# Performance work log

Measured on AMD Instinct MI355X. Metric: run time of the kernel, lower is better.

## Reference

```python
import jax, jax.numpy as jnp
import numpy as np

NUM_HEADS = 16
D_MODEL = 1024
HEAD_DIM = D_MODEL // NUM_HEADS
EPS = 1e-6


def setup_inputs() -> dict:
    key = jax.random.key(0)
    ks = jax.random.split(key, 9)
    B, S, D = 4, 8192, D_MODEL
    scale = 1.0 / np.sqrt(D)  # variance_scaling(1.0, fan_in, normal) approx
    inputs_q = jax.random.normal(ks[0], (B, S, D), dtype=jnp.float32)
    Wq = jax.random.normal(ks[1], (D, D), dtype=jnp.float32) * scale
    Wk = jax.random.normal(ks[2], (D, D), dtype=jnp.float32) * scale
    Wv = jax.random.normal(ks[3], (D, D), dtype=jnp.float32) * scale
    Wo = jax.random.normal(ks[4], (D, D), dtype=jnp.float32) * scale
    bq = jnp.zeros((D,), jnp.float32)
    bk = jnp.zeros((D,), jnp.float32)
    bv = jnp.zeros((D,), jnp.float32)
    bo = jnp.zeros((D,), jnp.float32)
    return {"inputs_q": inputs_q, "Wq": Wq, "bq": bq, "Wk": Wk, "bk": bk,
            "Wv": Wv, "bv": bv, "Wo": Wo, "bo": bo}


def _feature_map(x):
    return jax.nn.elu(x) + 1.0


def reference(inputs_q, Wq, bq, Wk, bk, Wv, bv, Wo, bo):
    B, S, D = inputs_q.shape
    H, Dh = NUM_HEADS, HEAD_DIM
    # QKV projections (self-attention: k,v inputs default to q input)
    q = (inputs_q @ Wq + bq).reshape(B, S, H, Dh)
    k = (inputs_q @ Wk + bk).reshape(B, S, H, Dh)
    v = (inputs_q @ Wv + bv).reshape(B, S, H, Dh)
    q = _feature_map(q)
    k = _feature_map(k)
    # KV outer-product accumulation: [B, H, Dh, Dh]
    kv = jnp.einsum('bkhd,bkhm->bhdm', k, v)
    out = jnp.einsum('bqhd,bhdm->bqhm', q, kv)
    # normalizer: q . sum_k(k)
    normalizer = jnp.einsum('bqhd,bkhd->bqh', q, k)
    normalizer = jnp.maximum(normalizer, EPS)
    out = out / normalizer[..., None]
    out = out.reshape(B, S, D)
    return out @ Wo + bo
```

## Files before the change

kernel.cpp:

```cpp
#include <hip/hip_runtime.h>
#include <cstdint>
#include <cstddef>

#define D_MODEL 1024
#define SEQ 8192

typedef __bf16  bf16x8 __attribute__((ext_vector_type(8)));
typedef short   short8 __attribute__((ext_vector_type(8)));
typedef float   f32x4  __attribute__((ext_vector_type(4)));
typedef unsigned short ushort_t;

__device__ __forceinline__ ushort_t f2bf(float f) {
  uint32_t u = __builtin_bit_cast(uint32_t, f);
  u += 0x7FFFu + ((u >> 16) & 1u);
  return (ushort_t)(u >> 16);
}
__device__ __forceinline__ void gll16(const void* g, void* l) {
  __builtin_amdgcn_global_load_lds(
      (const __attribute__((address_space(1))) void*)g,
      (__attribute__((address_space(3))) void*)l, 16, 0, 0);
}

__global__ void k_convert_x(const float* __restrict__ x, ushort_t* __restrict__ xb, int n) {
  int i = (blockIdx.x * 256 + threadIdx.x) * 8;
  if (i >= n) return;
  float4 v0 = *(const float4*)(x + i);
  float4 v1 = *(const float4*)(x + i + 4);
  ushort_t o[8] = { f2bf(v0.x), f2bf(v0.y), f2bf(v0.z), f2bf(v0.w),
                    f2bf(v1.x), f2bf(v1.y), f2bf(v1.z), f2bf(v1.w) };
  *(short8*)(xb + i) = *(const short8*)o;
}

__global__ void k_transpose_w(const float* W0, const float* W1, const float* W2, const float* W3,
                              ushort_t* Tqkv, ushort_t* To) {
  const float* src; ushort_t* dst;
  switch (blockIdx.z) {
    case 0: src = W0; dst = Tqkv; break;
    case 1: src = W1; dst = Tqkv + (size_t)1024 * 1024; break;
    case 2: src = W2; dst = Tqkv + (size_t)2048 * 1024; break;
    default: src = W3; dst = To; break;
  }
  __shared__ float tile[64][65];
  int tx = threadIdx.x;
  int c = tx & 63, r0 = tx >> 6;
  int bx = blockIdx.x * 64, by = blockIdx.y * 64;
  #pragma unroll
  for (int i = 0; i < 16; i++) {
    int r = i * 4 + r0;
    tile[r][c] = src[(size_t)(by + r) * D_MODEL + bx + c];
  }
  __syncthreads();
  #pragma unroll
  for (int i = 0; i < 16; i++) {
    int r = i * 4 + r0;
    dst[(size_t)(bx + r) * D_MODEL + by + c] = f2bf(tile[c][r]);
  }
}

template<int MODE, int NY>
__global__ __launch_bounds__(256) void k_gemm(const ushort_t* __restrict__ A,
                                              const ushort_t* __restrict__ Bt,
                                              const float* __restrict__ b0,
                                              const float* __restrict__ b1,
                                              const float* __restrict__ b2,
                                              ushort_t* __restrict__ o0,
                                              ushort_t* __restrict__ o1,
                                              ushort_t* __restrict__ o2,
                                              float* __restrict__ outf) {
  constexpr int SMEM_BYTES = (MODE == 2) ? 33792 : 32768;
  __shared__ __align__(16) char smem[SMEM_BYTES];
  ushort_t* As = (ushort_t*)smem;
  ushort_t* Bs = (ushort_t*)(smem + 8192);

  const int bid = blockIdx.x;
  const int xb = bid / NY;
  const int yb = bid % NY;
  const int m0 = xb * 128;
  const int n0 = yb * 128;

  const int tid = threadIdx.x;
  const int ln = tid & 63;
  const int w = tid >> 6;
  const int wr = (w >> 1) * 64, wc = (w & 1) * 64;

  const int lr = tid >> 2;
  const int kg = (tid & 3) * 8;
  const ushort_t* gA0 = A + (size_t)(m0 + lr) * D_MODEL + kg;
  const ushort_t* gA1 = gA0 + (size_t)64 * D_MODEL;
  const ushort_t* gB0 = Bt + (size_t)(n0 + lr) * D_MODEL + kg;
  const ushort_t* gB1 = gB0 + (size_t)64 * D_MODEL;

  const int wb = __builtin_amdgcn_readfirstlane(w);
  ushort_t* lA0 = As + wb * 512;
  ushort_t* lA1 = As + 2048 + wb * 512;
  ushort_t* lB0 = Bs + wb * 512;
  ushort_t* lB1 = Bs + 2048 + wb * 512;

  f32x4 acc[4][4];
  #pragma unroll
  for (int i = 0; i < 4; i++)
    #pragma unroll
    for (int j = 0; j < 4; j++) acc[i][j] = (f32x4){0.f, 0.f, 0.f, 0.f};

  const int ar = ln & 15;
  const int aq = (ln >> 4) * 8;

  for (int kt = 0; kt < D_MODEL / 32; kt++) {
    gll16(gA0, lA0); gll16(gA1, lA1);
    gll16(gB0, lB0); gll16(gB1, lB1);
    gA0 += 32; gA1 += 32; gB0 += 32; gB1 += 32;
    __syncthreads();
    bf16x8 a[4], b[4];
    #pragma unroll
    for (int i = 0; i < 4; i++) a[i] = *(const bf16x8*)&As[(wr + i * 16 + ar) * 32 + aq];
    #pragma unroll
    for (int j = 0; j < 4; j++) b[j] = *(const bf16x8*)&Bs[(wc + j * 16 + ar) * 32 + aq];
    #pragma unroll
    for (int i = 0; i < 4; i++)
      #pragma unroll
      for (int j = 0; j < 4; j++)
        acc[i][j] = __builtin_amdgcn_mfma_f32_16x16x32_bf16(a[i], b[j], acc[i][j], 0, 0, 0);
    __syncthreads();
  }

  const int colb = ln & 15;
  const int rowb = (ln >> 4) * 4;

  if (MODE == 0) {
    const int region = yb >> 3;
    const int nl0 = (yb & 7) * 128;
    const float* bias = region == 0 ? b0 : (region == 1 ? b1 : b2);
    ushort_t* gout    = region == 0 ? o0 : (region == 1 ? o1 : o2);
    const bool act = region < 2;
    ushort_t* Cs = (ushort_t*)smem;
    #pragma unroll
    for (int j = 0; j < 4; j++) {
      const int col = wc + j * 16 + colb;
      const float bv_ = bias[nl0 + col];
      #pragma unroll
      for (int i = 0; i < 4; i++) {
        const int rbase = wr + i * 16 + rowb;
        #pragma unroll
        for (int r = 0; r < 4; r++) {
          float v = acc[i][j][r] + bv_;
          if (act) v = (v > 0.f) ? v + 1.f : __expf(v);
          const int row = rbase + r;
          const int cg = col >> 3, co = col & 7;
          Cs[row * 128 + (((cg ^ (row & 15))) << 3) + co] = f2bf(v);
        }
      }
    }
    __syncthreads();
    #pragma unroll
    for (int c = 0; c < 8; c++) {
      const int idx = c * 256 + tid;
      const int row = idx >> 4, cg = idx & 15;
      short8 t = *(const short8*)&Cs[row * 128 + ((cg ^ (row & 15)) << 3)];
      *(short8*)&gout[(size_t)(m0 + row) * D_MODEL + nl0 + cg * 8] = t;
    }
  } else {
    float* Cf = (float*)smem;
    #pragma unroll
    for (int h = 0; h < 2; h++) {
      if (h) __syncthreads();
      if ((wr >> 6) == h) {
        #pragma unroll
        for (int j = 0; j < 4; j++) {
          const int col = wc + j * 16 + colb;
          const float bv_ = b0[n0 + col];
          #pragma unroll
          for (int i = 0; i < 4; i++) {
            const int rl = i * 16 + rowb;
            #pragma unroll
            for (int r = 0; r < 4; r++)
              Cf[(rl + r) * 132 + col] = acc[i][j][r] + bv_;
          }
        }
      }
      __syncthreads();
      #pragma unroll
      for (int c = 0; c < 8; c++) {
        const int idx = c * 256 + tid;
        const int row = idx >> 5, cg = idx & 31;
        float4 t = *(const float4*)&Cf[row * 132 + cg * 4];
        *(float4*)&outf[(size_t)(m0 + h * 64 + row) * D_MODEL + n0 + cg * 4] = t;
      }
    }
  }
}

__global__ __launch_bounds__(256) void k_kv_partial(const ushort_t* __restrict__ kmat,
                                                    const ushort_t* __restrict__ vmat,
                                                    float* __restrict__ part) {
  __shared__ __align__(16) ushort_t sbuf[4][2][2][512];
  const int tid = threadIdx.x, ln = tid & 63, w = tid >> 6;
  const int wb = __builtin_amdgcn_readfirstlane(w);
  const int bh = blockIdx.y, chunk = blockIdx.x;
  const int b = bh >> 4, h = bh & 15;
  const size_t cbase = ((size_t)b * SEQ + chunk * 1024 + w * 256) * D_MODEL + h * 64;
  const ushort_t* gk = kmat + cbase + (size_t)(ln >> 3) * D_MODEL + (ln & 7) * 8;
  const ushort_t* gv = vmat + cbase + (size_t)(ln >> 3) * D_MODEL + (ln & 7) * 8;

  float acc[8][8];
  float ksum[8];
  #pragma unroll
  for (int i = 0; i < 8; i++) { ksum[i] = 0.f;
    #pragma unroll
    for (int j = 0; j < 8; j++) acc[i][j] = 0.f; }

  const int r8 = (ln >> 3) * 8, c8 = (ln & 7) * 8;
  gll16(gk, &sbuf[wb][0][0][0]);
  gll16(gv, &sbuf[wb][0][1][0]);
  gk += 8 * D_MODEL; gv += 8 * D_MODEL;

  for (int bt = 0; bt < 32; bt++) {
    const int p = bt & 1;
    if (bt < 31) {
      gll16(gk, &sbuf[wb][p ^ 1][0][0]);
      gll16(gv, &sbuf[wb][p ^ 1][1][0]);
      gk += 8 * D_MODEL; gv += 8 * D_MODEL;
      __builtin_amdgcn_s_waitcnt(0x0F72);
    } else {
      __builtin_amdgcn_s_waitcnt(0x0F70);
    }
    #pragma unroll
    for (int s = 0; s < 8; s++) {
      short8 kk = *(const short8*)&sbuf[wb][p][0][s * 64 + r8];
      short8 vv = *(const short8*)&sbuf[wb][p][1][s * 64 + c8];
      float ka[8], va[8];
      #pragma unroll
      for (int i = 0; i < 8; i++) {
        ka[i] = __builtin_bit_cast(float, (uint32_t)(ushort_t)kk[i] << 16);
        va[i] = __builtin_bit_cast(float, (uint32_t)(ushort_t)vv[i] << 16);
      }
      #pragma unroll
      for (int i = 0; i < 8; i++) {
        ksum[i] += ka[i];
        #pragma unroll
        for (int j = 0; j < 8; j++) acc[i][j] += ka[i] * va[j];
      }
    }
  }
  float* p0 = part + ((size_t)bh * 32 + chunk * 4 + w) * 4160;
  #pragma unroll
  for (int i = 0; i < 8; i++)
    #pragma unroll
    for (int j = 0; j < 8; j++) p0[(r8 + i) * 64 + c8 + j] = acc[i][j];
  if ((ln & 7) == 0) {
    #pragma unroll
    for (int i = 0; i < 8; i++) p0[4096 + r8 + i] = ksum[i];
  }
}

__global__ void k_kv_reduce(const float* __restrict__ part, ushort_t* __restrict__ kvt) {
  const int bh = blockIdx.x, tid = threadIdx.x;
  const float* p0 = part + (size_t)bh * 32 * 4160;
  for (int idx = tid; idx < 4160; idx += 256) {
    float s = 0.f;
    #pragma unroll 4
    for (int c = 0; c < 32; c++) s += p0[(size_t)c * 4160 + idx];
    ushort_t bf = f2bf(s);
    if (idx < 4096) { int d = idx >> 6, m = idx & 63; kvt[(size_t)bh * 4160 + m * 64 + d] = bf; }
    else            { kvt[(size_t)bh * 4160 + 4096 + (idx - 4096)] = bf; }
  }
}

__global__ __launch_bounds__(256) void k_attn(const ushort_t* __restrict__ qmat,
                                              const ushort_t* __restrict__ kvt,
                                              ushort_t* __restrict__ attn) {
  __shared__ __align__(16) ushort_t kvs[65 * 80];
  __shared__ __align__(16) ushort_t qs[4][64 * 80];
  const int tid = threadIdx.x, ln = tid & 63, w = tid >> 6;
  const int bh = blockIdx.y, b = bh >> 4, h = bh & 15;

  for (int idx = tid; idx < 4160; idx += 256) {
    int m = idx >> 6, d = idx & 63;
    kvs[m * 80 + d] = kvt[(size_t)bh * 4160 + idx];
  }
  const size_t s0 = (size_t)b * SEQ + blockIdx.x * 256 + w * 64;
  #pragma unroll
  for (int c = 0; c < 8; c++) {
    int f = c * 64 + ln;
    int row = f >> 3, dg = (f & 7) * 8;
    short8 t = *(const short8*)&qmat[(s0 + row) * D_MODEL + h * 64 + dg];
    *(short8*)&qs[w][row * 80 + dg] = t;
  }
  __syncthreads();

  const int ar = ln & 15, aq = (ln >> 4) * 8;
  f32x4 acc[4][4], nacc[4];
  #pragma unroll
  for (int i = 0; i < 4; i++) { nacc[i] = (f32x4){0.f, 0.f, 0.f, 0.f};
    #pragma unroll
    for (int j = 0; j < 4; j++) acc[i][j] = (f32x4){0.f, 0.f, 0.f, 0.f}; }

  #pragma unroll
  for (int kk = 0; kk < 2; kk++) {
    const int ko = kk * 32 + aq;
    bf16x8 a[4], bb[4], bn;
    #pragma unroll
    for (int i = 0; i < 4; i++) a[i] = *(const bf16x8*)&qs[w][(i * 16 + ar) * 80 + ko];
    #pragma unroll
    for (int j = 0; j < 4; j++) bb[j] = *(const bf16x8*)&kvs[(j * 16 + ar) * 80 + ko];
    bn = *(const bf16x8*)&kvs[64 * 80 + ko];
    #pragma unroll
    for (int i = 0; i < 4; i++) {
      #pragma unroll
      for (int j = 0; j < 4; j++)
        acc[i][j] = __builtin_amdgcn_mfma_f32_16x16x32_bf16(a[i], bb[j], acc[i][j], 0, 0, 0);
      nacc[i] = __builtin_amdgcn_mfma_f32_16x16x32_bf16(a[i], bn, nacc[i], 0, 0, 0);
    }
  }

  const int colb = ln & 15, rowb = (ln >> 4) * 4;
  #pragma unroll
  for (int i = 0; i < 4; i++) {
    #pragma unroll
    for (int r = 0; r < 4; r++) {
      const int row = i * 16 + rowb + r;
      float nm = fmaxf(nacc[i][r], 1e-6f);
      float inv = 1.0f / nm;
      const size_t grow = s0 + row;
      #pragma unroll
      for (int j = 0; j < 4; j++) {
        float v = acc[i][j][r] * inv;
        attn[grow * D_MODEL + h * 64 + j * 16 + colb] = f2bf(v);
      }
    }
  }
}

extern "C" void kernel_launch(void* const* d_in, const int* in_sizes, int n_in,
                              void* d_out, int out_size, void* d_ws, size_t ws_size,
                              hipStream_t stream) {
  const float* x  = (const float*)d_in[0];
  const float* Wq = (const float*)d_in[1];
  const float* bq = (const float*)d_in[2];
  const float* Wk = (const float*)d_in[3];
  const float* bk = (const float*)d_in[4];
  const float* Wv = (const float*)d_in[5];
  const float* bv = (const float*)d_in[6];
  const float* Wo = (const float*)d_in[7];
  const float* bo = (const float*)d_in[8];
  float* out = (float*)d_out;

  const int M = in_sizes[0] / D_MODEL;
  const int B = M / SEQ;
  const int BH = B * 16;

  char* ws = (char*)d_ws;
  size_t off = 0;
  auto alloc = [&](size_t bytes) { char* p = ws + off; off += (bytes + 255) & ~(size_t)255; return p; };
  const size_t mb = (size_t)M * D_MODEL * 2;
  ushort_t* xb    = (ushort_t*)alloc(mb);
  ushort_t* qb    = (ushort_t*)alloc(mb);
  ushort_t* kb    = (ushort_t*)alloc(mb);
  ushort_t* vb    = (ushort_t*)alloc(mb);
  ushort_t* attnb = (ushort_t*)alloc(mb);
  ushort_t* wqkvt = (ushort_t*)alloc((size_t)3 * D_MODEL * D_MODEL * 2);
  ushort_t* wot   = (ushort_t*)alloc((size_t)D_MODEL * D_MODEL * 2);
  ushort_t* kvt   = (ushort_t*)alloc((size_t)BH * 4160 * 2);
  float*    part  = (float*)   alloc((size_t)BH * 32 * 4160 * 4);
  (void)ws_size; (void)n_in; (void)out_size;

  const int n = M * D_MODEL;
  k_convert_x<<<n / (256 * 8), 256, 0, stream>>>(x, xb, n);
  k_transpose_w<<<dim3(16, 16, 4), 256, 0, stream>>>(Wq, Wk, Wv, Wo, wqkvt, wot);

  k_gemm<0, 24><<<(M / 128) * 24, 256, 0, stream>>>(xb, wqkvt, bq, bk, bv, qb, kb, vb, nullptr);

  k_kv_partial<<<dim3(8, BH), 256, 0, stream>>>(kb, vb, part);
  k_kv_reduce<<<BH, 256, 0, stream>>>(part, kvt);
  k_attn<<<dim3(SEQ / 256, BH), 256, 0, stream>>>(qb, kvt, attnb);

  k_gemm<2, 8><<<(M / 128) * 8, 256, 0, stream>>>(attnb, wot, bo, nullptr, nullptr, nullptr, nullptr, nullptr, out);
}
```

Baseline: 742.6 us.

## Rewrite GEMM as 256x256 tile, 8-wave double-buffered pipelined kernel

```diff
diff --git a/kernel.cpp b/kernel.cpp
--- a/kernel.cpp
+++ b/kernel.cpp
@@ -19,6 +19,10 @@
   __builtin_amdgcn_global_load_lds(
       (const __attribute__((address_space(1))) void*)g,
       (__attribute__((address_space(3))) void*)l, 16, 0, 0);
+}
+__device__ __forceinline__ void stage_half(const ushort_t* g, char* l0) {
+  gll16(g, l0);
+  gll16(g + 65536, l0 + 8192);
 }
 
 __global__ void k_convert_x(const float* __restrict__ x, ushort_t* __restrict__ xb, int n) {
@@ -58,132 +62,167 @@
 }
 
 template<int MODE, int NY>
-__global__ __launch_bounds__(256) void k_gemm(const ushort_t* __restrict__ A,
-                                              const ushort_t* __restrict__ Bt,
-                                              const float* __restrict__ b0,
-                                              const float* __restrict__ b1,
-                                              const float* __restrict__ b2,
-                                              ushort_t* __restrict__ o0,
-                                              ushort_t* __restrict__ o1,
-                                              ushort_t* __restrict__ o2,
-                                              float* __restrict__ outf) {
-  constexpr int SMEM_BYTES = (MODE == 2) ? 33792 : 32768;
-  __shared__ __align__(16) char smem[SMEM_BYTES];
-  ushort_t* As = (ushort_t*)smem;
-  ushort_t* Bs = (ushort_t*)(smem + 8192);
-
-  const int bid = blockIdx.x;
-  const int xb = bid / NY;
-  const int yb = bid % NY;
-  const int m0 = xb * 128;
-  const int n0 = yb * 128;
+__global__ __launch_bounds__(512, 2) void k_gemm(const ushort_t* __restrict__ A,
+                                                 const ushort_t* __restrict__ Bt,
+                                                 const float* __restrict__ b0,
+                                                 const float* __restrict__ b1,
+                                                 const float* __restrict__ b2,
+                                                 ushort_t* __restrict__ o0,
+                                                 ushort_t* __restrict__ o1,
+                                                 ushort_t* __restrict__ o2,
+                                                 float* __restrict__ outf) {
+  __shared__ __align__(16) char smem[131072];
+
+  const int nwg = gridDim.x;
+  const int bid0 = blockIdx.x;
+  const int bid = (bid0 & 7) * (nwg >> 3) + (bid0 >> 3);
+  const int xb = bid / NY, yb = bid % NY;
+  const int m0 = xb * 256, n0 = yb * 256;
 
   const int tid = threadIdx.x;
   const int ln = tid & 63;
-  const int w = tid >> 6;
-  const int wr = (w >> 1) * 64, wc = (w & 1) * 64;
-
-  const int lr = tid >> 2;
-  const int kg = (tid & 3) * 8;
-  const ushort_t* gA0 = A + (size_t)(m0 + lr) * D_MODEL + kg;
-  const ushort_t* gA1 = gA0 + (size_t)64 * D_MODEL;
-  const ushort_t* gB0 = Bt + (size_t)(n0 + lr) * D_MODEL + kg;
-  const ushort_t* gB1 = gB0 + (size_t)64 * D_MODEL;
-
+  const int w  = tid >> 6;
   const int wb = __builtin_amdgcn_readfirstlane(w);
-  ushort_t* lA0 = As + wb * 512;
-  ushort_t* lA1 = As + 2048 + wb * 512;
-  ushort_t* lB0 = Bs + wb * 512;
-  ushort_t* lB1 = Bs + 2048 + wb * 512;
-
-  f32x4 acc[4][4];
-  #pragma unroll
-  for (int i = 0; i < 4; i++)
+  const int wm = wb >> 2, wn = wb & 3;
+
+  const int srow = wb * 8 + (ln >> 3);
+  const int schk = ((ln & 7) ^ ((ln >> 3) & 7)) * 8;
+  const ushort_t* gA = A  + (size_t)(m0 + srow) * D_MODEL + schk;
+  const ushort_t* gB = Bt + (size_t)(n0 + srow) * D_MODEL + schk;
+
+#define STAGE_A(BUF, H, T) stage_half(gA + (size_t)(T) * 64 + (size_t)(H) * 131072, (BUF) + (H) * 16384 + wb * 1024)
+#define STAGE_B(BUF, H, T) stage_half(gB + (size_t)(T) * 64 + (size_t)(H) * 131072, (BUF) + 32768 + (H) * 16384 + wb * 1024)
+
+  char* cur = smem;
+  char* nxt = smem + 65536;
+  STAGE_B(cur, 0, 0); STAGE_B(cur, 1, 0); STAGE_A(cur, 0, 0); STAGE_A(cur, 1, 0);
+  STAGE_B(nxt, 0, 1); STAGE_B(nxt, 1, 1); STAGE_A(nxt, 0, 1);
+  asm volatile("s_waitcnt vmcnt(6)" ::: "memory");
+  __builtin_amdgcn_s_barrier();
+
+  f32x4 acc[8][4];
+  #pragma unroll
+  for (int i = 0; i < 8; i++)
     #pragma unroll
     for (int j = 0; j < 4; j++) acc[i][j] = (f32x4){0.f, 0.f, 0.f, 0.f};
-
-  const int ar = ln & 15;
-  const int aq = (ln >> 4) * 8;
-
-  for (int kt = 0; kt < D_MODEL / 32; kt++) {
-    gll16(gA0, lA0); gll16(gA1, lA1);
-    gll16(gB0, lB0); gll16(gB1, lB1);
-    gA0 += 32; gA1 += 32; gB0 += 32; gB1 += 32;
-    __syncthreads();
-    bf16x8 a[4], b[4];
-    #pragma unroll
-    for (int i = 0; i < 4; i++) a[i] = *(const bf16x8*)&As[(wr + i * 16 + ar) * 32 + aq];
-    #pragma unroll
-    for (int j = 0; j < 4; j++) b[j] = *(const bf16x8*)&Bs[(wc + j * 16 + ar) * 32 + aq];
-    #pragma unroll
-    for (int i = 0; i < 4; i++)
-      #pragma unroll
-      for (int j = 0; j < 4; j++)
-        acc[i][j] = __builtin_amdgcn_mfma_f32_16x16x32_bf16(a[i], b[j], acc[i][j], 0, 0, 0);
-    __syncthreads();
-  }
-
-  const int colb = ln & 15;
-  const int rowb = (ln >> 4) * 4;
-
-  if (MODE == 0) {
-    const int region = yb >> 3;
-    const int nl0 = (yb & 7) * 128;
+  bf16x8 fa[4][2], fb0[2][2], fb1[2][2];
+
+  const int ar  = ln & 15;
+  const int cw0 = (((ln >> 4)    ) ^ (ln & 7)) << 4;
+  const int cw1 = (((ln >> 4) + 4) ^ (ln & 7)) << 4;
+  const int arow = wm * 128 + ar;
+  const int brow = wn * 64 + ar;
+
+#define LDA(MH) { _Pragma("unroll") for (int mi = 0; mi < 4; ++mi) { \
+    const char* p_ = cur + ((arow + (MH) * 64 + mi * 16) << 7); \
+    fa[mi][0] = *(const bf16x8*)(p_ + cw0); fa[mi][1] = *(const bf16x8*)(p_ + cw1); } }
+#define LDB(FB, NH) { _Pragma("unroll") for (int nj = 0; nj < 2; ++nj) { \
+    const char* p_ = cur + 32768 + ((brow + (NH) * 32 + nj * 16) << 7); \
+    FB[nj][0] = *(const bf16x8*)(p_ + cw0); FB[nj][1] = *(const bf16x8*)(p_ + cw1); } }
+#define QUAD(MH, NH, FB) { _Pragma("unroll") for (int mi = 0; mi < 4; ++mi) \
+    _Pragma("unroll") for (int nj = 0; nj < 2; ++nj) { \
+      acc[(MH)*4+mi][(NH)*2+nj] = __builtin_amdgcn_mfma_f32_16x16x32_bf16(fa[mi][0], FB[nj][0], acc[(MH)*4+mi][(NH)*2+nj], 0, 0, 0); \
+      acc[(MH)*4+mi][(NH)*2+nj] = __builtin_amdgcn_mfma_f32_16x16x32_bf16(fa[mi][1], FB[nj][1], acc[(MH)*4+mi][(NH)*2+nj], 0, 0, 0); } }
+#define PHASE_SYNC { __builtin_amdgcn_s_barrier(); \
+                     asm volatile("s_waitcnt lgkmcnt(0)" ::: "memory"); \
+                     __builtin_amdgcn_sched_barrier(0); }
+
+  #pragma unroll 2
+  for (int kt = 0; kt < 16; ++kt) {
+    const bool st1 = (kt + 1 < 16);
+    const bool st2 = (kt + 2 < 16);
+    LDA(0); LDB(fb0, 0);
+    if (st1) STAGE_A(nxt, 1, kt + 1);
+    PHASE_SYNC;
+    __builtin_amdgcn_s_setprio(1); QUAD(0, 0, fb0); __builtin_amdgcn_s_setprio(0);
+    __builtin_amdgcn_s_barrier();
+    LDB(fb1, 1);
+    PHASE_SYNC;
+    __builtin_amdgcn_s_setprio(1); QUAD(0, 1, fb1); __builtin_amdgcn_s_setprio(0);
+    __builtin_amdgcn_s_barrier();
+    LDA(1);
+    if (st2) STAGE_B(cur, 0, kt + 2);
+    PHASE_SYNC;
+    __builtin_amdgcn_s_setprio(1); QUAD(1, 1, fb1); __builtin_amdgcn_s_setprio(0);
+    __builtin_amdgcn_s_barrier();
+    if (st2) { STAGE_B(cur, 1, kt + 2); STAGE_A(cur, 0, kt + 2); }
+    __builtin_amdgcn_s_barrier();
+    __builtin_amdgcn_s_setprio(1); QUAD(1, 0, fb0); __builtin_amdgcn_s_setprio(0);
+    if (kt < 14)       asm volatile("s_waitcnt vmcnt(6)" ::: "memory");
+    else if (kt == 14) asm volatile("s_waitcnt vmcnt(0)" ::: "memory");
+    __builtin_amdgcn_s_barrier();
+    char* t_ = cur; cur = nxt; nxt = t_;
+  }
+#undef STAGE_A
+#undef STAGE_B
+#undef LDA
+#undef LDB
+#undef QUAD
+#undef PHASE_SYNC
+
+  const int colb = ln & 15, rowb = (ln >> 4) * 4;
+
+  if constexpr (MODE == 0) {
+    const int region = yb >> 2;
+    const int nl0 = (yb & 3) * 256;
     const float* bias = region == 0 ? b0 : (region == 1 ? b1 : b2);
     ushort_t* gout    = region == 0 ? o0 : (region == 1 ? o1 : o2);
     const bool act = region < 2;
     ushort_t* Cs = (ushort_t*)smem;
     #pragma unroll
-    for (int j = 0; j < 4; j++) {
-      const int col = wc + j * 16 + colb;
+    for (int j = 0; j < 4; ++j) {
+      const int col = wn * 64 + j * 16 + colb;
       const float bv_ = bias[nl0 + col];
       #pragma unroll
-      for (int i = 0; i < 4; i++) {
-        const int rbase = wr + i * 16 + rowb;
+      for (int i = 0; i < 8; ++i) {
+        const int rb_ = wm * 128 + i * 16 + rowb;
         #pragma unroll
-        for (int r = 0; r < 4; r++) {
+        for (int r = 0; r < 4; ++r) {
           float v = acc[i][j][r] + bv_;
           if (act) v = (v > 0.f) ? v + 1.f : __expf(v);
-          const int row = rbase + r;
-          const int cg = col >> 3, co = col & 7;
-          Cs[row * 128 + (((cg ^ (row & 15))) << 3) + co] = f2bf(v);
+          const int row = rb_ + r;
+          const int ch = col >> 3;
+          Cs[row * 256 + ((ch ^ (row & 31)) << 3) + (col & 7)] = f2bf(v);
         }
       }
     }
     __syncthreads();
     #pragma unroll
-    for (int c = 0; c < 8; c++) {
-      const int idx = c * 256 + tid;
-      const int row = idx >> 4, cg = idx & 15;
-      short8 t = *(const short8*)&Cs[row * 128 + ((cg ^ (row & 15)) << 3)];
-      *(short8*)&gout[(size_t)(m0 + row) * D_MODEL + nl0 + cg * 8] = t;
+    for (int c = 0; c < 16; ++c) {
+      const int idx = c * 512 + tid;
+      const int row = idx >> 5, ch = idx & 31;
+      short8 t = *(const short8*)&Cs[row * 256 + ((ch ^ (row & 31)) << 3)];
+      *(short8*)&gout[(size_t)(m0 + row) * D_MODEL + nl0 + ch * 8] = t;
     }
   } else {
     float* Cf = (float*)smem;
     #pragma unroll
-    for (int h = 0; h < 2; h++) {
+    for (int h = 0; h < 2; ++h) {
       if (h) __syncthreads();
-      if ((wr >> 6) == h) {
+      if (wm == h) {
         #pragma unroll
-        for (int j = 0; j < 4; j++) {
-          const int col = wc + j * 16 + colb;
+        for (int j = 0; j < 4; ++j) {
+          const int col = wn * 64 + j * 16 + colb;
           const float bv_ = b0[n0 + col];
           #pragma unroll
-          for (int i = 0; i < 4; i++) {
+          for (int i = 0; i < 8; ++i) {
             const int rl = i * 16 + rowb;
             #pragma unroll
-            for (int r = 0; r < 4; r++)
-              Cf[(rl + r) * 132 + col] = acc[i][j][r] + bv_;
+            for (int r = 0; r < 4; ++r) {
+              const int row = rl + r;
+              const int ch = col >> 2;
+              Cf[row * 256 + ((ch ^ (row & 7)) << 2) + (col & 3)] = acc[i][j][r] + bv_;
+            }
           }
         }
       }
       __syncthreads();
       #pragma unroll
-      for (int c = 0; c < 8; c++) {
-        const int idx = c * 256 + tid;
-        const int row = idx >> 5, cg = idx & 31;
-        float4 t = *(const float4*)&Cf[row * 132 + cg * 4];
-        *(float4*)&outf[(size_t)(m0 + h * 64 + row) * D_MODEL + n0 + cg * 4] = t;
+      for (int c = 0; c < 16; ++c) {
+        const int idx = c * 512 + tid;
+        const int row = idx >> 6, ch = idx & 63;
+        float4 t = *(const float4*)&Cf[row * 256 + ((ch ^ (row & 7)) << 2)];
+        *(float4*)&outf[(size_t)(m0 + h * 128 + row) * D_MODEL + n0 + ch * 4] = t;
       }
     }
   }
@@ -367,11 +406,11 @@
   k_convert_x<<<n / (256 * 8), 256, 0, stream>>>(x, xb, n);
   k_transpose_w<<<dim3(16, 16, 4), 256, 0, stream>>>(Wq, Wk, Wv, Wo, wqkvt, wot);
 
-  k_gemm<0, 24><<<(M / 128) * 24, 256, 0, stream>>>(xb, wqkvt, bq, bk, bv, qb, kb, vb, nullptr);
+  k_gemm<0, 12><<<(M / 256) * 12, 512, 0, stream>>>(xb, wqkvt, bq, bk, bv, qb, kb, vb, nullptr);
 
   k_kv_partial<<<dim3(8, BH), 256, 0, stream>>>(kb, vb, part);
   k_kv_reduce<<<BH, 256, 0, stream>>>(part, kvt);
   k_attn<<<dim3(SEQ / 256, BH), 256, 0, stream>>>(qb, kvt, attnb);
 
-  k_gemm<2, 8><<<(M / 128) * 8, 256, 0, stream>>>(attnb, wot, bo, nullptr, nullptr, nullptr, nullptr, nullptr, out);
-}
+  k_gemm<2, 4><<<(M / 256) * 4, 512, 0, stream>>>(attnb, wot, bo, nullptr, nullptr, nullptr, nullptr, nullptr, out);
+}
```

Result: faster. 673.6 us (-9.3%).
